# Optimization experiments

Measured on AMD Instinct MI355X. Metric: run time of the kernel, lower is better.

## Reference

```python
import jax, jax.numpy as jnp
import numpy as np

D_MODEL = 1024
NUM_HEADS = 16
DEPTH = D_MODEL // NUM_HEADS
B, S = 4, 2048


def setup_inputs() -> dict:
    key = jax.random.key(0)
    ks = jax.random.split(key, 13)
    sd = 1.0 / np.sqrt(D_MODEL)
    inp = {
        "q_in": jax.random.normal(ks[0], (B, S, D_MODEL), jnp.float32),
        "k_in": jax.random.normal(ks[1], (B, S, D_MODEL), jnp.float32),
        "v_in": jax.random.normal(ks[2], (B, S, D_MODEL), jnp.float32),
        # binary padding/causal-style mask: 1 = masked position
        "m_in": (jax.random.uniform(ks[3], (B, 1, S, S)) < 0.1).astype(jnp.float32),
        "Wq": jax.random.normal(ks[4], (D_MODEL, D_MODEL), jnp.float32) * sd,
        "bq": jax.random.normal(ks[5], (D_MODEL,), jnp.float32) * 0.01,
        "Wk": jax.random.normal(ks[6], (D_MODEL, D_MODEL), jnp.float32) * sd,
        "bk": jax.random.normal(ks[7], (D_MODEL,), jnp.float32) * 0.01,
        "Wv": jax.random.normal(ks[8], (D_MODEL, D_MODEL), jnp.float32) * sd,
        "bv": jax.random.normal(ks[9], (D_MODEL,), jnp.float32) * 0.01,
        "Wo": jax.random.normal(ks[10], (D_MODEL, D_MODEL), jnp.float32) * sd,
        "bo": jax.random.normal(ks[11], (D_MODEL,), jnp.float32) * 0.01,
    }
    return inp


def _split(t):
    # [B,S,D] -> [B,H,S,depth]
    b, s, _ = t.shape
    return t.reshape(b, s, NUM_HEADS, DEPTH).transpose(0, 2, 1, 3)


def reference(q_in, k_in, v_in, m_in, Wq, bq, Wk, bk, Wv, bv, Wo, bo):
    # torch Linear: x @ W^T + b
    q = _split(q_in @ Wq.T + bq)
    k = _split(k_in @ Wk.T + bk)
    v = _split(v_in @ Wv.T + bv)
    scale = jnp.sqrt(jnp.asarray(DEPTH, jnp.float32))
    scores = jnp.einsum("bhqd,bhkd->bhqk", q, k) / scale
    scores = scores - m_in * 1e6
    attn = jax.nn.softmax(scores, axis=-1)
    out = jnp.einsum("bhqk,bhkd->bhqd", attn, v)  # [B,H,S,depth]
    out = out.transpose(0, 2, 1, 3).reshape(q_in.shape[0], -1, D_MODEL)
    return out @ Wo.T + bo
```

## Files before the change

kernel.cpp:

```cpp
#include <hip/hip_runtime.h>


typedef __bf16 bf16_t;
typedef __bf16 bf16x8 __attribute__((ext_vector_type(8)));
typedef float floatx4 __attribute__((ext_vector_type(4)));

#define DMODEL 1024
#define NHEAD  16
#define DEPTH  64
#define BATCH  4
#define SEQ    2048
#define MROWS  (BATCH * SEQ)

#define QSCALE 0.18033688011112042f

#define GLDS16(gaddr, laddr)                                                   \
  __builtin_amdgcn_global_load_lds(                                            \
      (__attribute__((address_space(1))) void*)(gaddr),                        \
      (__attribute__((address_space(3))) void*)(laddr), 16, 0, 0)

__global__ __launch_bounds__(256) void cvt_weights(
    const float* __restrict__ w0, const float* __restrict__ w1,
    const float* __restrict__ w2, const float* __restrict__ w3,
    bf16_t* __restrict__ out) {
  const int n_per4 = (DMODEL * DMODEL) / 4;
  int idx = blockIdx.x * blockDim.x + threadIdx.x;
  int t = idx / n_per4;
  int e4 = idx - t * n_per4;
  const float* src = (t == 0) ? w0 : (t == 1) ? w1 : (t == 2) ? w2 : w3;
  const float sc = (t == 0) ? QSCALE : 1.0f;
  float4 v = ((const float4*)src)[e4];
  bf16_t* dst = out + (size_t)t * (DMODEL * DMODEL) + (size_t)e4 * 4;
  dst[0] = (bf16_t)(v.x * sc); dst[1] = (bf16_t)(v.y * sc);
  dst[2] = (bf16_t)(v.z * sc); dst[3] = (bf16_t)(v.w * sc);
}

__global__ __launch_bounds__(256) void mask_prepack(
    const float* __restrict__ m, unsigned int* __restrict__ M32) {
  size_t t = (size_t)blockIdx.x * blockDim.x + threadIdx.x;
  int lane = t & 63;
  int it = (t >> 6) & 31;
  int g  = (t >> 11) & 63;
  int b  = (int)(t >> 17);
  int quad = lane >> 4, l16 = lane & 15;
  unsigned int bits = 0;
#pragma unroll
  for (int mi = 0; mi < 2; mi++) {
#pragma unroll
    for (int r = 0; r < 4; r++) {
      const int q = g * 32 + mi * 16 + quad * 4 + r;
      const float* row = m + ((size_t)b * SEQ + q) * SEQ + it * 64 + l16;
#pragma unroll
      for (int ni = 0; ni < 4; ni++) {
        if (row[ni * 16] == 0.f) bits |= 1u << ((mi * 4 + r) * 4 + ni);
      }
    }
  }
  M32[t] = bits;
}

template <bool A32, int OMODE>
__global__ __launch_bounds__(256) void gemm128(
    const void* __restrict__ Av, const bf16_t* __restrict__ Bt,
    const float* __restrict__ bias, float bias_scale, void* __restrict__ Ov,
    int M, int N, int K) {
  __shared__ __align__(16) char AsRaw[A32 ? 128 * 32 * 4 : 128 * 32 * 2];
  __shared__ __align__(16) bf16_t Bs[128 * 32];
  const int tid = threadIdx.x;
  const int lane = tid & 63;
  const int w = tid >> 6;
  const int quad = lane >> 4;
  const int l16 = lane & 15;
  const int wm = w & 1, wn = w >> 1;

  const int lin = blockIdx.x + 8 * blockIdx.y;
  const int c = lin & 7;
  const int j = lin >> 3;
  const int n0 = (j & 7) * 128;
  const int m0 = ((j >> 3) * 8 + c) * 128;

  const int r4 = lane >> 2;
  const int c4 = (lane & 3) ^ (r4 & 3);
  const bf16_t* Bg = Bt + (size_t)(n0 + w * 32 + r4) * K + c4 * 8;
  char* BsB = (char*)Bs + (w * 32) * 64;

  const int r8 = lane >> 3;
  const int c8 = (lane & 7) ^ r8;
  const float*  Ag32 = (const float*)Av + (size_t)(m0 + w * 32 + r8) * K + c8 * 4;
  const bf16_t* Ag16 = (const bf16_t*)Av + (size_t)(m0 + w * 32 + r4) * K + c4 * 8;
  char* AsB32 = AsRaw + (w * 32) * 128;
  char* AsB16 = AsRaw + (w * 32) * 64;

  floatx4 acc[4][4] = {};

  for (int kk = 0; kk < K; kk += 32) {
    __syncthreads();
    if (A32) {
#pragma unroll
      for (int jj = 0; jj < 4; jj++)
        GLDS16(Ag32 + kk + (size_t)jj * 8 * K, AsB32 + jj * 8 * 128);
    } else {
      GLDS16(Ag16 + kk, AsB16);
      GLDS16(Ag16 + kk + (size_t)16 * K, AsB16 + 16 * 64);
    }
    GLDS16(Bg + kk, BsB);
    GLDS16(Bg + kk + (size_t)16 * K, BsB + 16 * 64);
    __syncthreads();

    bf16x8 af[4], bfr[4];
#pragma unroll
    for (int mi = 0; mi < 4; mi++) {
      const int mrow = wm * 64 + mi * 16 + l16;
      if (A32) {
        const char* Arow = AsRaw + mrow * 128;
        const int sw = l16 & 7;
        float4 f0 = *(const float4*)(Arow + (((2 * quad) ^ sw) * 16));
        float4 f1 = *(const float4*)(Arow + (((2 * quad + 1) ^ sw) * 16));
        bf16x8 a;
        a[0] = (bf16_t)f0.x; a[1] = (bf16_t)f0.y; a[2] = (bf16_t)f0.z; a[3] = (bf16_t)f0.w;
        a[4] = (bf16_t)f1.x; a[5] = (bf16_t)f1.y; a[6] = (bf16_t)f1.z; a[7] = (bf16_t)f1.w;
        af[mi] = a;
      } else {
        const char* Arow = AsRaw + mrow * 64;
        af[mi] = *(const bf16x8*)(Arow + ((quad ^ (l16 & 3)) * 16));
      }
    }
#pragma unroll
    for (int ni = 0; ni < 4; ni++) {
      const char* Brow = (const char*)Bs + (wn * 64 + ni * 16 + l16) * 64;
      bfr[ni] = *(const bf16x8*)(Brow + ((quad ^ (l16 & 3)) * 16));
    }
#pragma unroll
    for (int mi = 0; mi < 4; mi++)
#pragma unroll
      for (int ni = 0; ni < 4; ni++)
        acc[mi][ni] = __builtin_amdgcn_mfma_f32_16x16x32_bf16(af[mi], bfr[ni], acc[mi][ni], 0, 0, 0);
  }

#pragma unroll
  for (int ni = 0; ni < 4; ni++) {
    const int col = n0 + wn * 64 + ni * 16 + l16;
    const float bv = bias_scale * bias[col];
#pragma unroll
    for (int mi = 0; mi < 4; mi++) {
#pragma unroll
      for (int r = 0; r < 4; r++) {
        const int row = m0 + wm * 64 + mi * 16 + quad * 4 + r;
        const float val = acc[mi][ni][r] + bv;
        if (OMODE == 0) {
          const int b = row >> 11, s = row & (SEQ - 1);
          const int h = col >> 6, d = col & (DEPTH - 1);
          ((bf16_t*)Ov)[((((size_t)b * NHEAD + h) * SEQ + s) << 6) + d] = (bf16_t)val;
        } else if (OMODE == 1) {
          const int b = row >> 11, s = row & (SEQ - 1);
          const int h = col >> 6, d = col & (DEPTH - 1);
          ((bf16_t*)Ov)[(((size_t)b * NHEAD + h) * DEPTH + d) * SEQ + s] = (bf16_t)val;
        } else {
          ((float*)Ov)[(size_t)row * N + col] = val;
        }
      }
    }
  }
}

__global__ __launch_bounds__(256) void attn_kernel(
    const bf16_t* __restrict__ Qh, const bf16_t* __restrict__ Kh,
    const bf16_t* __restrict__ Vt, const unsigned int* __restrict__ M32,
    bf16_t* __restrict__ O) {
  const int lane = threadIdx.x & 63;
  const int w = __builtin_amdgcn_readfirstlane(threadIdx.x >> 6);
  const int quad = lane >> 4;
  const int l16 = lane & 15;

  const int lin = blockIdx.x + 16 * blockIdx.y + 256 * blockIdx.z;
  const int x8 = lin & 7;
  const int kk = lin >> 3;
  const int qt = kk & 15;
  const int p = ((kk >> 4) << 3) | x8;
  const int h = p & 15;
  const int b = p >> 4;
  const int q0 = qt * 128;

  const bf16_t* Qb = Qh + ((size_t)b * NHEAD + h) * SEQ * DEPTH;
  const bf16_t* Kb = Kh + ((size_t)b * NHEAD + h) * SEQ * DEPTH;
  const bf16_t* Vb = Vt + ((size_t)b * NHEAD + h) * DEPTH * SEQ;
  const unsigned int* Mw =
      M32 + ((size_t)b * 64 + (qt * 4 + w)) * 32 * 64 + lane;

  __shared__ __align__(16) bf16_t Ksm[64 * 64];
  __shared__ __align__(16) bf16_t Vsm[64 * 64];
  __shared__ __align__(16) bf16_t Pw[4][32][72];

  const int r8 = lane >> 3;
  const int c8 = (lane & 7) ^ r8;
  const bf16_t* Kg = Kb + (size_t)(w * 16 + r8) * DEPTH + c8 * 8;
  const bf16_t* Vg = Vb + (size_t)(w * 16 + r8) * SEQ + c8 * 8;
  char* KsB = (char*)Ksm + (w * 16) * 128;
  char* VsB = (char*)Vsm + (w * 16) * 128;

  bf16x8 aq[2][2];
#pragma unroll
  for (int mi = 0; mi < 2; mi++) {
    const bf16_t* qp = Qb + (size_t)(q0 + w * 32 + mi * 16 + l16) * DEPTH + quad * 8;
    aq[mi][0] = *(const bf16x8*)qp;
    aq[mi][1] = *(const bf16x8*)(qp + 32);
  }

  floatx4 acco[2][4] = {};
  float lsum[2][4] = {};
  const int swz = l16 & 7;

  for (int it = 0; it < SEQ / 64; ++it) {
    const int sk = it * 64;
    __syncthreads();
    GLDS16(Kg + (size_t)sk * DEPTH, KsB);
    GLDS16(Kg + (size_t)sk * DEPTH + 8 * DEPTH, KsB + 8 * 128);
    GLDS16(Vg + sk, VsB);
    GLDS16(Vg + sk + (size_t)8 * SEQ, VsB + 8 * 128);
    __syncthreads();

    const unsigned int mword = Mw[it * 64];

#pragma unroll
    for (int ni = 0; ni < 4; ni++) {
      const char* Krow = (const char*)Ksm + (ni * 16 + l16) * 128;
      bf16x8 k0 = *(const bf16x8*)(Krow + ((quad ^ swz) * 16));
      bf16x8 k1 = *(const bf16x8*)(Krow + (((4 + quad) ^ swz) * 16));
      floatx4 s[2] = {};
#pragma unroll
      for (int mi = 0; mi < 2; mi++) {
        s[mi] = __builtin_amdgcn_mfma_f32_16x16x32_bf16(aq[mi][0], k0, s[mi], 0, 0, 0);
        s[mi] = __builtin_amdgcn_mfma_f32_16x16x32_bf16(aq[mi][1], k1, s[mi], 0, 0, 0);
      }
#pragma unroll
      for (int mi = 0; mi < 2; mi++) {
#pragma unroll
        for (int r = 0; r < 4; r++) {
          float pv = __builtin_amdgcn_exp2f(s[mi][r]);
          const int idx = (mi * 4 + r) * 4 + ni;
          const int km = ((int)(mword << (31 - idx))) >> 31;
          pv = __int_as_float(__float_as_int(pv) & km);
          lsum[mi][r] += pv;
          Pw[w][mi * 16 + quad * 4 + r][ni * 16 + l16] = (bf16_t)pv;
        }
      }
    }

    bf16x8 pa[2][2];
#pragma unroll
    for (int mi = 0; mi < 2; mi++)
#pragma unroll
      for (int kb = 0; kb < 2; kb++)
        pa[mi][kb] = *(const bf16x8*)(&Pw[w][mi * 16 + l16][kb * 32 + quad * 8]);
#pragma unroll
    for (int ni = 0; ni < 4; ni++) {
      const char* Vrow = (const char*)Vsm + (ni * 16 + l16) * 128;
#pragma unroll
      for (int kb = 0; kb < 2; kb++) {
        bf16x8 vb = *(const bf16x8*)(Vrow + ((((kb * 4) + quad) ^ swz) * 16));
#pragma unroll
        for (int mi = 0; mi < 2; mi++)
          acco[mi][ni] = __builtin_amdgcn_mfma_f32_16x16x32_bf16(pa[mi][kb], vb, acco[mi][ni], 0, 0, 0);
      }
    }
  }

  float inv_l[2][4];
#pragma unroll
  for (int mi = 0; mi < 2; mi++)
#pragma unroll
    for (int r = 0; r < 4; r++) {
      float s = lsum[mi][r];
      s += __shfl_xor(s, 1);
      s += __shfl_xor(s, 2);
      s += __shfl_xor(s, 4);
      s += __shfl_xor(s, 8);
      inv_l[mi][r] = __frcp_rn(s);
    }

#pragma unroll
  for (int mi = 0; mi < 2; mi++)
#pragma unroll
    for (int ni = 0; ni < 4; ni++)
#pragma unroll
      for (int r = 0; r < 4; r++) {
        const int s = q0 + w * 32 + mi * 16 + quad * 4 + r;
        const int d = h * DEPTH + ni * 16 + l16;
        O[((size_t)b * SEQ + s) * DMODEL + d] = (bf16_t)(acco[mi][ni][r] * inv_l[mi][r]);
      }
}

extern "C" void kernel_launch(void* const* d_in, const int* in_sizes, int n_in,
                              void* d_out, int out_size, void* d_ws, size_t ws_size,
                              hipStream_t stream) {
  const float* q_in = (const float*)d_in[0];
  const float* k_in = (const float*)d_in[1];
  const float* v_in = (const float*)d_in[2];
  const float* m_in = (const float*)d_in[3];
  const float* Wq = (const float*)d_in[4];
  const float* bq = (const float*)d_in[5];
  const float* Wk = (const float*)d_in[6];
  const float* bk = (const float*)d_in[7];
  const float* Wv = (const float*)d_in[8];
  const float* bv = (const float*)d_in[9];
  const float* Wo = (const float*)d_in[10];
  const float* bo = (const float*)d_in[11];

  char* ws = (char*)d_ws;
  const size_t MB = 1024 * 1024;
  bf16_t* wbf = (bf16_t*)ws;
  bf16_t* Wq_bf = wbf + 0 * (size_t)DMODEL * DMODEL;
  bf16_t* Wk_bf = wbf + 1 * (size_t)DMODEL * DMODEL;
  bf16_t* Wv_bf = wbf + 2 * (size_t)DMODEL * DMODEL;
  bf16_t* Wo_bf = wbf + 3 * (size_t)DMODEL * DMODEL;
  bf16_t* Qh   = (bf16_t*)(ws + 8 * MB);
  bf16_t* Kh   = (bf16_t*)(ws + 24 * MB);
  bf16_t* Vth  = (bf16_t*)(ws + 40 * MB);
  bf16_t* Obuf = (bf16_t*)(ws + 56 * MB);
  unsigned int* M32 = (unsigned int*)(ws + 72 * MB);

  cvt_weights<<<(4 * (DMODEL * DMODEL / 4)) / 256, 256, 0, stream>>>(
      Wq, Wk, Wv, Wo, wbf);
  mask_prepack<<<(BATCH * 64 * 32 * 64) / 256, 256, 0, stream>>>(m_in, M32);

  dim3 gg(DMODEL / 128, MROWS / 128);
  gemm128<true, 0><<<gg, 256, 0, stream>>>(q_in, Wq_bf, bq, QSCALE, Qh, MROWS, DMODEL, DMODEL);
  gemm128<true, 0><<<gg, 256, 0, stream>>>(k_in, Wk_bf, bk, 1.0f, Kh, MROWS, DMODEL, DMODEL);
  gemm128<true, 1><<<gg, 256, 0, stream>>>(v_in, Wv_bf, bv, 1.0f, Vth, MROWS, DMODEL, DMODEL);

  dim3 ga(SEQ / 128, NHEAD, BATCH);
  attn_kernel<<<ga, 256, 0, stream>>>(Qh, Kh, Vth, M32, Obuf);

  gemm128<false, 2><<<gg, 256, 0, stream>>>(Obuf, Wo_bf, bo, 1.0f, d_out, MROWS, DMODEL, DMODEL);
}
```

Before: 451.8 us.

## Pre-convert activations to bf16 and double attention query tile per block

```diff
diff --git a/kernel.cpp b/kernel.cpp
--- a/kernel.cpp
+++ b/kernel.cpp
@@ -2,6 +2,7 @@
 
 
 typedef __bf16 bf16_t;
+typedef __bf16 bf16x4 __attribute__((ext_vector_type(4)));
 typedef __bf16 bf16x8 __attribute__((ext_vector_type(8)));
 typedef float floatx4 __attribute__((ext_vector_type(4)));
 
@@ -35,6 +36,17 @@
   dst[2] = (bf16_t)(v.z * sc); dst[3] = (bf16_t)(v.w * sc);
 }
 
+__global__ __launch_bounds__(256) void cvt_one(
+    const float* __restrict__ src, bf16_t* __restrict__ dst) {
+  size_t i = (size_t)blockIdx.x * blockDim.x + threadIdx.x;
+  const float4* s = (const float4*)(src + i * 8);
+  float4 f0 = s[0], f1 = s[1];
+  bf16x8 o;
+  o[0] = (bf16_t)f0.x; o[1] = (bf16_t)f0.y; o[2] = (bf16_t)f0.z; o[3] = (bf16_t)f0.w;
+  o[4] = (bf16_t)f1.x; o[5] = (bf16_t)f1.y; o[6] = (bf16_t)f1.z; o[7] = (bf16_t)f1.w;
+  *(bf16x8*)(dst + i * 8) = o;
+}
+
 __global__ __launch_bounds__(256) void mask_prepack(
     const float* __restrict__ m, unsigned int* __restrict__ M32) {
   size_t t = (size_t)blockIdx.x * blockDim.x + threadIdx.x;
@@ -59,12 +71,12 @@
   M32[t] = bits;
 }
 
-template <bool A32, int OMODE>
+template <int OMODE>
 __global__ __launch_bounds__(256) void gemm128(
-    const void* __restrict__ Av, const bf16_t* __restrict__ Bt,
+    const bf16_t* __restrict__ A, const bf16_t* __restrict__ Bt,
     const float* __restrict__ bias, float bias_scale, void* __restrict__ Ov,
     int M, int N, int K) {
-  __shared__ __align__(16) char AsRaw[A32 ? 128 * 32 * 4 : 128 * 32 * 2];
+  __shared__ __align__(16) bf16_t As[128 * 32];
   __shared__ __align__(16) bf16_t Bs[128 * 32];
   const int tid = threadIdx.x;
   const int lane = tid & 63;
@@ -81,28 +93,17 @@
 
   const int r4 = lane >> 2;
   const int c4 = (lane & 3) ^ (r4 & 3);
+  const bf16_t* Ag = A + (size_t)(m0 + w * 32 + r4) * K + c4 * 8;
   const bf16_t* Bg = Bt + (size_t)(n0 + w * 32 + r4) * K + c4 * 8;
+  char* AsB = (char*)As + (w * 32) * 64;
   char* BsB = (char*)Bs + (w * 32) * 64;
-
-  const int r8 = lane >> 3;
-  const int c8 = (lane & 7) ^ r8;
-  const float*  Ag32 = (const float*)Av + (size_t)(m0 + w * 32 + r8) * K + c8 * 4;
-  const bf16_t* Ag16 = (const bf16_t*)Av + (size_t)(m0 + w * 32 + r4) * K + c4 * 8;
-  char* AsB32 = AsRaw + (w * 32) * 128;
-  char* AsB16 = AsRaw + (w * 32) * 64;
 
   floatx4 acc[4][4] = {};
 
   for (int kk = 0; kk < K; kk += 32) {
     __syncthreads();
-    if (A32) {
-#pragma unroll
-      for (int jj = 0; jj < 4; jj++)
-        GLDS16(Ag32 + kk + (size_t)jj * 8 * K, AsB32 + jj * 8 * 128);
-    } else {
-      GLDS16(Ag16 + kk, AsB16);
-      GLDS16(Ag16 + kk + (size_t)16 * K, AsB16 + 16 * 64);
-    }
+    GLDS16(Ag + kk, AsB);
+    GLDS16(Ag + kk + (size_t)16 * K, AsB + 16 * 64);
     GLDS16(Bg + kk, BsB);
     GLDS16(Bg + kk + (size_t)16 * K, BsB + 16 * 64);
     __syncthreads();
@@ -110,20 +111,8 @@
     bf16x8 af[4], bfr[4];
 #pragma unroll
     for (int mi = 0; mi < 4; mi++) {
-      const int mrow = wm * 64 + mi * 16 + l16;
-      if (A32) {
-        const char* Arow = AsRaw + mrow * 128;
-        const int sw = l16 & 7;
-        float4 f0 = *(const float4*)(Arow + (((2 * quad) ^ sw) * 16));
-        float4 f1 = *(const float4*)(Arow + (((2 * quad + 1) ^ sw) * 16));
-        bf16x8 a;
-        a[0] = (bf16_t)f0.x; a[1] = (bf16_t)f0.y; a[2] = (bf16_t)f0.z; a[3] = (bf16_t)f0.w;
-        a[4] = (bf16_t)f1.x; a[5] = (bf16_t)f1.y; a[6] = (bf16_t)f1.z; a[7] = (bf16_t)f1.w;
-        af[mi] = a;
-      } else {
-        const char* Arow = AsRaw + mrow * 64;
-        af[mi] = *(const bf16x8*)(Arow + ((quad ^ (l16 & 3)) * 16));
-      }
+      const char* Arow = (const char*)As + (wm * 64 + mi * 16 + l16) * 64;
+      af[mi] = *(const bf16x8*)(Arow + ((quad ^ (l16 & 3)) * 16));
     }
 #pragma unroll
     for (int ni = 0; ni < 4; ni++) {
@@ -172,24 +161,25 @@
   const int quad = lane >> 4;
   const int l16 = lane & 15;
 
-  const int lin = blockIdx.x + 16 * blockIdx.y + 256 * blockIdx.z;
-  const int x8 = lin & 7;
-  const int kk = lin >> 3;
-  const int qt = kk & 15;
-  const int p = ((kk >> 4) << 3) | x8;
+  const int lin = blockIdx.x + 8 * (blockIdx.y + 16 * blockIdx.z);
+  const int c = lin & 7;
+  const int j = lin >> 3;
+  const int p = (j & 7) * 8 + c;
+  const int qt = j >> 3;
   const int h = p & 15;
   const int b = p >> 4;
-  const int q0 = qt * 128;
+  const int q0 = qt * 256;
 
   const bf16_t* Qb = Qh + ((size_t)b * NHEAD + h) * SEQ * DEPTH;
   const bf16_t* Kb = Kh + ((size_t)b * NHEAD + h) * SEQ * DEPTH;
   const bf16_t* Vb = Vt + ((size_t)b * NHEAD + h) * DEPTH * SEQ;
-  const unsigned int* Mw =
-      M32 + ((size_t)b * 64 + (qt * 4 + w)) * 32 * 64 + lane;
+  const unsigned int* Mw0 =
+      M32 + ((size_t)b * 64 + (qt * 8 + w * 2)) * 32 * 64 + lane;
+  const unsigned int* Mw1 = Mw0 + 32 * 64;
 
   __shared__ __align__(16) bf16_t Ksm[64 * 64];
   __shared__ __align__(16) bf16_t Vsm[64 * 64];
-  __shared__ __align__(16) bf16_t Pw[4][32][72];
+  __shared__ __align__(16) bf16_t Pw[4][64][68];
 
   const int r8 = lane >> 3;
   const int c8 = (lane & 7) ^ r8;
@@ -198,16 +188,16 @@
   char* KsB = (char*)Ksm + (w * 16) * 128;
   char* VsB = (char*)Vsm + (w * 16) * 128;
 
-  bf16x8 aq[2][2];
-#pragma unroll
-  for (int mi = 0; mi < 2; mi++) {
-    const bf16_t* qp = Qb + (size_t)(q0 + w * 32 + mi * 16 + l16) * DEPTH + quad * 8;
+  bf16x8 aq[4][2];
+#pragma unroll
+  for (int mi = 0; mi < 4; mi++) {
+    const bf16_t* qp = Qb + (size_t)(q0 + w * 64 + mi * 16 + l16) * DEPTH + quad * 8;
     aq[mi][0] = *(const bf16x8*)qp;
     aq[mi][1] = *(const bf16x8*)(qp + 32);
   }
 
-  floatx4 acco[2][4] = {};
-  float lsum[2][4] = {};
+  floatx4 acco[4][4] = {};
+  float lsum[4][4] = {};
   const int swz = l16 & 7;
 
   for (int it = 0; it < SEQ / 64; ++it) {
@@ -219,25 +209,29 @@
     GLDS16(Vg + sk + (size_t)8 * SEQ, VsB + 8 * 128);
     __syncthreads();
 
-    const unsigned int mword = Mw[it * 64];
+    const unsigned int mw0 = Mw0[it * 64];
+    const unsigned int mw1 = Mw1[it * 64];
 
 #pragma unroll
     for (int ni = 0; ni < 4; ni++) {
       const char* Krow = (const char*)Ksm + (ni * 16 + l16) * 128;
       bf16x8 k0 = *(const bf16x8*)(Krow + ((quad ^ swz) * 16));
       bf16x8 k1 = *(const bf16x8*)(Krow + (((4 + quad) ^ swz) * 16));
-      floatx4 s[2] = {};
-#pragma unroll
-      for (int mi = 0; mi < 2; mi++) {
-        s[mi] = __builtin_amdgcn_mfma_f32_16x16x32_bf16(aq[mi][0], k0, s[mi], 0, 0, 0);
-        s[mi] = __builtin_amdgcn_mfma_f32_16x16x32_bf16(aq[mi][1], k1, s[mi], 0, 0, 0);
-      }
-#pragma unroll
-      for (int mi = 0; mi < 2; mi++) {
+      floatx4 s[4];
+#pragma unroll
+      for (int mi = 0; mi < 4; mi++) {
+        floatx4 z = {};
+        z = __builtin_amdgcn_mfma_f32_16x16x32_bf16(aq[mi][0], k0, z, 0, 0, 0);
+        s[mi] = __builtin_amdgcn_mfma_f32_16x16x32_bf16(aq[mi][1], k1, z, 0, 0, 0);
+      }
+#pragma unroll
+      for (int mi = 0; mi < 4; mi++) {
+        const unsigned int mword = (mi < 2) ? mw0 : mw1;
+        const int mb = (mi & 1) * 16;
 #pragma unroll
         for (int r = 0; r < 4; r++) {
           float pv = __builtin_amdgcn_exp2f(s[mi][r]);
-          const int idx = (mi * 4 + r) * 4 + ni;
+          const int idx = mb + r * 4 + ni;
           const int km = ((int)(mword << (31 - idx))) >> 31;
           pv = __int_as_float(__float_as_int(pv) & km);
           lsum[mi][r] += pv;
@@ -246,12 +240,17 @@
       }
     }
 
-    bf16x8 pa[2][2];
-#pragma unroll
-    for (int mi = 0; mi < 2; mi++)
-#pragma unroll
-      for (int kb = 0; kb < 2; kb++)
-        pa[mi][kb] = *(const bf16x8*)(&Pw[w][mi * 16 + l16][kb * 32 + quad * 8]);
+    bf16x8 pa[4][2];
+#pragma unroll
+    for (int mi = 0; mi < 4; mi++) {
+#pragma unroll
+      for (int kb = 0; kb < 2; kb++) {
+        const bf16_t* pp = &Pw[w][mi * 16 + l16][kb * 32 + quad * 8];
+        bf16x4 lo = *(const bf16x4*)pp;
+        bf16x4 hi = *(const bf16x4*)(pp + 4);
+        pa[mi][kb] = __builtin_shufflevector(lo, hi, 0, 1, 2, 3, 4, 5, 6, 7);
+      }
+    }
 #pragma unroll
     for (int ni = 0; ni < 4; ni++) {
       const char* Vrow = (const char*)Vsm + (ni * 16 + l16) * 128;
@@ -259,15 +258,15 @@
       for (int kb = 0; kb < 2; kb++) {
         bf16x8 vb = *(const bf16x8*)(Vrow + ((((kb * 4) + quad) ^ swz) * 16));
 #pragma unroll
-        for (int mi = 0; mi < 2; mi++)
+        for (int mi = 0; mi < 4; mi++)
           acco[mi][ni] = __builtin_amdgcn_mfma_f32_16x16x32_bf16(pa[mi][kb], vb, acco[mi][ni], 0, 0, 0);
       }
     }
   }
 
-  float inv_l[2][4];
-#pragma unroll
-  for (int mi = 0; mi < 2; mi++)
+  float inv_l[4][4];
+#pragma unroll
+  for (int mi = 0; mi < 4; mi++)
 #pragma unroll
     for (int r = 0; r < 4; r++) {
       float s = lsum[mi][r];
@@ -279,12 +278,12 @@
     }
 
 #pragma unroll
-  for (int mi = 0; mi < 2; mi++)
+  for (int mi = 0; mi < 4; mi++)
 #pragma unroll
     for (int ni = 0; ni < 4; ni++)
 #pragma unroll
       for (int r = 0; r < 4; r++) {
-        const int s = q0 + w * 32 + mi * 16 + quad * 4 + r;
+        const int s = q0 + w * 64 + mi * 16 + quad * 4 + r;
         const int d = h * DEPTH + ni * 16 + l16;
         O[((size_t)b * SEQ + s) * DMODEL + d] = (bf16_t)(acco[mi][ni][r] * inv_l[mi][r]);
       }
@@ -313,10 +312,11 @@
   bf16_t* Wk_bf = wbf + 1 * (size_t)DMODEL * DMODEL;
   bf16_t* Wv_bf = wbf + 2 * (size_t)DMODEL * DMODEL;
   bf16_t* Wo_bf = wbf + 3 * (size_t)DMODEL * DMODEL;
-  bf16_t* Qh   = (bf16_t*)(ws + 8 * MB);
-  bf16_t* Kh   = (bf16_t*)(ws + 24 * MB);
-  bf16_t* Vth  = (bf16_t*)(ws + 40 * MB);
-  bf16_t* Obuf = (bf16_t*)(ws + 56 * MB);
+  bf16_t* Abf  = (bf16_t*)(ws + 8 * MB);
+  bf16_t* Obuf = (bf16_t*)(ws + 8 * MB);
+  bf16_t* Qh   = (bf16_t*)(ws + 24 * MB);
+  bf16_t* Kh   = (bf16_t*)(ws + 40 * MB);
+  bf16_t* Vth  = (bf16_t*)(ws + 56 * MB);
   unsigned int* M32 = (unsigned int*)(ws + 72 * MB);
 
   cvt_weights<<<(4 * (DMODEL * DMODEL / 4)) / 256, 256, 0, stream>>>(
@@ -324,12 +324,17 @@
   mask_prepack<<<(BATCH * 64 * 32 * 64) / 256, 256, 0, stream>>>(m_in, M32);
 
   dim3 gg(DMODEL / 128, MROWS / 128);
-  gemm128<true, 0><<<gg, 256, 0, stream>>>(q_in, Wq_bf, bq, QSCALE, Qh, MROWS, DMODEL, DMODEL);
-  gemm128<true, 0><<<gg, 256, 0, stream>>>(k_in, Wk_bf, bk, 1.0f, Kh, MROWS, DMODEL, DMODEL);
-  gemm128<true, 1><<<gg, 256, 0, stream>>>(v_in, Wv_bf, bv, 1.0f, Vth, MROWS, DMODEL, DMODEL);
-
-  dim3 ga(SEQ / 128, NHEAD, BATCH);
+  const int cvt_blocks = (MROWS * DMODEL / 8) / 256;
+
+  cvt_one<<<cvt_blocks, 256, 0, stream>>>(q_in, Abf);
+  gemm128<0><<<gg, 256, 0, stream>>>(Abf, Wq_bf, bq, QSCALE, Qh, MROWS, DMODEL, DMODEL);
+  cvt_one<<<cvt_blocks, 256, 0, stream>>>(k_in, Abf);
+  gemm128<0><<<gg, 256, 0, stream>>>(Abf, Wk_bf, bk, 1.0f, Kh, MROWS, DMODEL, DMODEL);
+  cvt_one<<<cvt_blocks, 256, 0, stream>>>(v_in, Abf);
+  gemm128<1><<<gg, 256, 0, stream>>>(Abf, Wv_bf, bv, 1.0f, Vth, MROWS, DMODEL, DMODEL);
+
+  dim3 ga(SEQ / 256, NHEAD, BATCH);
   attn_kernel<<<ga, 256, 0, stream>>>(Qh, Kh, Vth, M32, Obuf);
 
-  gemm128<false, 2><<<gg, 256, 0, stream>>>(Obuf, Wo_bf, bo, 1.0f, d_out, MROWS, DMODEL, DMODEL);
-}
+  gemm128<2><<<gg, 256, 0, stream>>>(Obuf, Wo_bf, bo, 1.0f, d_out, MROWS, DMODEL, DMODEL);
+}
```

New measurement: 497.0 us. 1.1x slower.
